# Optimization experiments

Hardware: AMD Instinct MI355X
Metric: run time of the kernel (lower is better)

## Reference

```python
import jax, jax.numpy as jnp
import numpy as np

N, E = 100000, 1600000
F_IN, H, HG, L, C = 128, 128, 128, 3, 40


def setup_inputs() -> dict:
    key = jax.random.key(0)
    ks = jax.random.split(key, 12)
    s = 0.05
    return dict(
        x=jax.random.normal(ks[0], (N, F_IN), jnp.float32),
        edge_index=jax.random.randint(ks[1], (2, E), 0, N),
        edge_weight=jax.random.uniform(ks[2], (E,), jnp.float32),
        h0=jax.random.normal(ks[3], (N, HG), jnp.float32),
        linW=jax.random.normal(ks[4], (F_IN, H), jnp.float32) * s,
        linB=jnp.zeros((H,), jnp.float32),
        convW=jax.random.normal(ks[5], (L, H, H), jnp.float32) * s,
        convB=jnp.zeros((L, H), jnp.float32),
        gru_Wih=jax.random.normal(ks[6], (3 * HG, H), jnp.float32) * s,
        gru_Whh=jax.random.normal(ks[7], (3 * HG, HG), jnp.float32) * s,
        gru_bih=jnp.zeros((3 * HG,), jnp.float32),
        gru_bhh=jnp.zeros((3 * HG,), jnp.float32),
        fcW=jax.random.normal(ks[8], (HG, C), jnp.float32) * s,
        fcB=jnp.zeros((C,), jnp.float32),
    )


def _gru(x, h, Wih, Whh, bih, bhh):
    # torch.nn.GRUCell math (gate order: r, z, n)
    gi = x @ Wih.T + bih  # [N, 3*HG]
    gh = h @ Whh.T + bhh  # [N, 3*HG]
    ir, iz, in_ = jnp.split(gi, 3, axis=-1)
    hr, hz, hn = jnp.split(gh, 3, axis=-1)
    r = jax.nn.sigmoid(ir + hr)
    z = jax.nn.sigmoid(iz + hz)
    n = jnp.tanh(in_ + r * hn)
    return (1.0 - z) * n + z * h


def _gcn_conv(x, src, dst, ew, W, b, n_nodes):
    # PyG GCNConv: linear -> symmetric-normalized sparse aggregation -> bias
    xw = x @ W  # [N, H]
    deg = jax.ops.segment_sum(ew, dst, num_segments=n_nodes)
    dinv = jnp.where(deg > 0, jax.lax.rsqrt(deg), 0.0)
    norm = dinv[src] * ew * dinv[dst]  # [E+N]
    msg = xw[src] * norm[:, None]      # gather + scale (irregular access)
    out = jax.ops.segment_sum(msg, dst, num_segments=n_nodes)  # scatter-add
    return out + b


def reference(x, edge_index, edge_weight, h0, linW, linB, convW, convB,
              gru_Wih, gru_Whh, gru_bih, gru_bhh, fcW, fcB):
    n_nodes = x.shape[0]
    # GCNConv default: add self-loops with weight 1 before normalization
    loops = jnp.arange(n_nodes)
    src = jnp.concatenate([edge_index[0], loops])
    dst = jnp.concatenate([edge_index[1], loops])
    ew = jnp.concatenate([edge_weight, jnp.ones((n_nodes,), edge_weight.dtype)])

    h = h0
    xh = jax.nn.relu(x @ linW + linB)
    h = _gru(xh, h, gru_Wih, gru_Whh, gru_bih, gru_bhh)
    for l in range(convW.shape[0]):  # fixed small layer count
        xh = jax.nn.relu(_gcn_conv(xh, src, dst, ew, convW[l], convB[l], n_nodes))
        h = _gru(xh, h, gru_Wih, gru_Whh, gru_bih, gru_bhh)
    return h @ fcW + fcB
```

## Files before the change

kernel.cpp:

```cpp
#include <hip/hip_runtime.h>
#include <hip/hip_bf16.h>
#include <math.h>

typedef __attribute__((ext_vector_type(8))) short bf8_t;
typedef __attribute__((ext_vector_type(4))) float f4_t;
typedef __attribute__((ext_vector_type(8))) unsigned short us8_t;

__device__ inline unsigned short f2bf(float f) {
  union { float f; unsigned u; } x; x.f = f;
  unsigned r = x.u + 0x7FFF + ((x.u >> 16) & 1);
  return (unsigned short)(r >> 16);
}
__device__ inline float bf2f(unsigned short b) {
  union { unsigned u; float f; } x; x.u = ((unsigned)b) << 16;
  return x.f;
}
__device__ inline float bflo(unsigned v) {
  union { unsigned u; float f; } x; x.u = v << 16; return x.f;
}
__device__ inline float bfhi(unsigned v) {
  union { unsigned u; float f; } x; x.u = v & 0xFFFF0000u; return x.f;
}

__device__ inline void async_copy16(const void* g, void* l) {
  __builtin_amdgcn_global_load_lds(
      (const __attribute__((address_space(1))) unsigned int*)g,
      (__attribute__((address_space(3))) unsigned int*)l, 16, 0, 0);
}


__global__ void k_fill1(float* __restrict__ p, int n) {
  int i = blockIdx.x * blockDim.x + threadIdx.x;
  if (i < n) p[i] = 1.0f;
}

__global__ void k_zero_i(int* __restrict__ p, int n) {
  int i = blockIdx.x * blockDim.x + threadIdx.x;
  if (i < n) p[i] = 0;
}

__global__ void k_scatter_deg(const int* __restrict__ dst, const float* __restrict__ ew,
                              float* __restrict__ deg, int E) {
  int e = blockIdx.x * blockDim.x + threadIdx.x;
  if (e < E) atomicAdd(&deg[dst[e]], ew[e]);
}

__global__ void k_count(const int* __restrict__ dst, int* __restrict__ cnt, int E) {
  int e = blockIdx.x * blockDim.x + threadIdx.x;
  if (e < E) atomicAdd(&cnt[dst[e]], 1);
}

__global__ void k_rsqrt(float* __restrict__ p, int n) {
  int i = blockIdx.x * blockDim.x + threadIdx.x;
  if (i < n) p[i] = rsqrtf(p[i]);
}

__global__ void k_f2bf(const float* __restrict__ in, unsigned short* __restrict__ out,
                       size_t n8) {
  size_t i = (size_t)blockIdx.x * blockDim.x + threadIdx.x;
  if (i >= n8) return;
  const float4* p = (const float4*)(in + i * 8);
  float4 a = p[0], b = p[1];
  us8_t v;
  v[0] = f2bf(a.x); v[1] = f2bf(a.y); v[2] = f2bf(a.z); v[3] = f2bf(a.w);
  v[4] = f2bf(b.x); v[5] = f2bf(b.y); v[6] = f2bf(b.z); v[7] = f2bf(b.w);
  *(us8_t*)(out + i * 8) = v;
}

__global__ void k_packB(const float* __restrict__ W, unsigned short* __restrict__ out,
                        int K, int Ncols, int ldw, int trans) {
  int idx = blockIdx.x * 256 + threadIdx.x;
  int total = (Ncols / 16) * (K / 32) * 64;
  if (idx >= total) return;
  int lane = idx & 63;
  int frag = idx >> 6;
  int kt = K / 32;
  int k0 = frag % kt;
  int n0 = frag / kt;
  int n = n0 * 16 + (lane & 15);
  int kbase = k0 * 32 + (lane >> 4) * 8;
  us8_t v;
#pragma unroll
  for (int j = 0; j < 8; ++j) {
    int k = kbase + j;
    float f = trans ? W[(size_t)n * ldw + k] : W[(size_t)k * ldw + n];
    v[j] = f2bf(f);
  }
  *(us8_t*)(out + (size_t)idx * 8) = v;
}


__global__ __launch_bounds__(256) void k_scan_block(
    const int* __restrict__ cnt, int* __restrict__ partial,
    int* __restrict__ bsum, int n) {
  __shared__ int s[256];
  int tid = threadIdx.x;
  int i = blockIdx.x * 256 + tid;
  s[tid] = (i < n) ? cnt[i] : 0;
  __syncthreads();
#pragma unroll
  for (int d = 1; d < 256; d <<= 1) {
    int t = (tid >= d) ? s[tid - d] : 0;
    __syncthreads();
    s[tid] += t;
    __syncthreads();
  }
  if (i < n) partial[i] = s[tid];
  if (tid == 255) bsum[blockIdx.x] = s[255];
}

__global__ __launch_bounds__(512) void k_scan_sums(int* __restrict__ bsum, int nb) {
  __shared__ int s[512];
  int tid = threadIdx.x;
  s[tid] = (tid < nb) ? bsum[tid] : 0;
  __syncthreads();
#pragma unroll
  for (int d = 1; d < 512; d <<= 1) {
    int t = (tid >= d) ? s[tid - d] : 0;
    __syncthreads();
    s[tid] += t;
    __syncthreads();
  }
  if (tid < nb) bsum[tid] = s[tid];
}

__global__ __launch_bounds__(256) void k_scan_add(
    const int* __restrict__ partial, const int* __restrict__ bsum,
    int* __restrict__ rowptr, int* __restrict__ cursor, int n) {
  int i = blockIdx.x * 256 + threadIdx.x;
  if (i == 0) { rowptr[0] = 0; cursor[0] = 0; }
  if (i < n) {
    int v = partial[i] + (blockIdx.x > 0 ? bsum[blockIdx.x - 1] : 0);
    rowptr[i + 1] = v;
    if (i + 1 < n) cursor[i + 1] = v;
  }
}

__global__ __launch_bounds__(256) void k_csr_fill(
    const int* __restrict__ src, const int* __restrict__ dst,
    const float* __restrict__ ew, const float* __restrict__ dinv,
    int* __restrict__ cursor, int2* __restrict__ csr, int E) {
  int e = blockIdx.x * 256 + threadIdx.x;
  if (e >= E) return;
  int s = src[e], d = dst[e];
  float w = dinv[s] * ew[e] * dinv[d];
  int pos = atomicAdd(&cursor[d], 1);
  csr[pos] = make_int2(s, __float_as_int(w));
}


template<bool RELU, bool BIAS>
__global__ __launch_bounds__(256) void k_mfma_gemm(
    const unsigned short* __restrict__ A, const unsigned short* __restrict__ Bp,
    const float* __restrict__ bias, unsigned short* __restrict__ C, int M) {
  __shared__ unsigned char smem[32 * 1024];
  int wave = threadIdx.x >> 6, lane = threadIdx.x & 63;
  int row0 = (blockIdx.x * 4 + wave) * 16;
  int m = lane & 15, q = lane >> 4;

#pragma unroll
  for (int i = 0; i < 8; ++i) {
    int f = wave * 8 + i;
    async_copy16((const unsigned char*)Bp + (size_t)f * 1024 + lane * 16,
                 smem + f * 1024);
  }
  __syncthreads();
  if (row0 >= M) return;

  int arow = row0 + m; if (arow >= M) arow = M - 1;
  bf8_t a[4];
#pragma unroll
  for (int k0 = 0; k0 < 4; ++k0)
    a[k0] = *(const bf8_t*)(A + (size_t)arow * 128 + k0 * 32 + q * 8);

#pragma unroll
  for (int n0 = 0; n0 < 8; ++n0) {
    f4_t acc = {};
#pragma unroll
    for (int k0 = 0; k0 < 4; ++k0) {
      bf8_t b = *(const bf8_t*)(smem + (n0 * 4 + k0) * 1024 + lane * 16);
      acc = __builtin_amdgcn_mfma_f32_16x16x32_bf16(a[k0], b, acc, 0, 0, 0);
    }
    int col = n0 * 16 + m;
    float bs = BIAS ? bias[col] : 0.f;
#pragma unroll
    for (int r = 0; r < 4; ++r) {
      int grow = row0 + q * 4 + r;
      if (grow < M) {
        float v = acc[r] + bs;
        if (RELU) v = fmaxf(v, 0.f);
        C[(size_t)grow * 128 + col] = f2bf(v);
      }
    }
  }
}


__global__ __launch_bounds__(256) void k_gru_mfma(
    const unsigned short* __restrict__ xh,
    const float* h_in,
    float* h_out,
    const unsigned short* __restrict__ Bi,
    const unsigned short* __restrict__ Bh,
    const float* __restrict__ bih, const float* __restrict__ bhh, int M) {
  __shared__ unsigned char smem[24 * 1024];
  int wave = threadIdx.x >> 6, lane = threadIdx.x & 63;
  int row0 = (blockIdx.x * 4 + wave) * 16;
  int m = lane & 15, q = lane >> 4;
  int arow = row0 + m; if (arow >= M) arow = M - 1;

  bf8_t ax[4], ah[4];
#pragma unroll
  for (int k0 = 0; k0 < 4; ++k0) {
    ax[k0] = *(const bf8_t*)(xh + (size_t)arow * 128 + k0 * 32 + q * 8);
    const float* hp = h_in + (size_t)arow * 128 + k0 * 32 + q * 8;
    float4 h0 = *(const float4*)hp;
    float4 h1 = *(const float4*)(hp + 4);
    bf8_t t;
    t[0] = (short)f2bf(h0.x); t[1] = (short)f2bf(h0.y);
    t[2] = (short)f2bf(h0.z); t[3] = (short)f2bf(h0.w);
    t[4] = (short)f2bf(h1.x); t[5] = (short)f2bf(h1.y);
    t[6] = (short)f2bf(h1.z); t[7] = (short)f2bf(h1.w);
    ah[k0] = t;
  }

  auto stage = [&](int g) {
#pragma unroll
    for (int s = 0; s < 6; ++s) {
      int cc = g + 8 * (s >= 3 ? s - 3 : s);
      const unsigned short* src = (s < 3) ? Bi : Bh;
      int f = s * 4 + wave;
      async_copy16((const unsigned char*)src + ((size_t)(cc * 4 + wave)) * 1024 + lane * 16,
                   smem + f * 1024);
    }
  };

  stage(0);
  for (int g = 0; g < 8; ++g) {
    __syncthreads();
    f4_t air = {}, aiz = {}, ain = {}, ahr = {}, ahz = {}, ahn = {};
#pragma unroll
    for (int k0 = 0; k0 < 4; ++k0) {
      bf8_t br = *(const bf8_t*)(smem + (0 * 4 + k0) * 1024 + lane * 16);
      bf8_t bz = *(const bf8_t*)(smem + (1 * 4 + k0) * 1024 + lane * 16);
      bf8_t bn = *(const bf8_t*)(smem + (2 * 4 + k0) * 1024 + lane * 16);
      bf8_t cr = *(const bf8_t*)(smem + (3 * 4 + k0) * 1024 + lane * 16);
      bf8_t cz = *(const bf8_t*)(smem + (4 * 4 + k0) * 1024 + lane * 16);
      bf8_t cn = *(const bf8_t*)(smem + (5 * 4 + k0) * 1024 + lane * 16);
      air = __builtin_amdgcn_mfma_f32_16x16x32_bf16(ax[k0], br, air, 0, 0, 0);
      aiz = __builtin_amdgcn_mfma_f32_16x16x32_bf16(ax[k0], bz, aiz, 0, 0, 0);
      ain = __builtin_amdgcn_mfma_f32_16x16x32_bf16(ax[k0], bn, ain, 0, 0, 0);
      ahr = __builtin_amdgcn_mfma_f32_16x16x32_bf16(ah[k0], cr, ahr, 0, 0, 0);
      ahz = __builtin_amdgcn_mfma_f32_16x16x32_bf16(ah[k0], cz, ahz, 0, 0, 0);
      ahn = __builtin_amdgcn_mfma_f32_16x16x32_bf16(ah[k0], cn, ahn, 0, 0, 0);
    }
    __syncthreads();
    if (g < 7) stage(g + 1);

    int col = g * 16 + m;
    float bir_ = bih[col], biz_ = bih[col + 128], bin_ = bih[col + 256];
    float bhr_ = bhh[col], bhz_ = bhh[col + 128], bhn_ = bhh[col + 256];
#pragma unroll
    for (int r = 0; r < 4; ++r) {
      int grow = row0 + q * 4 + r;
      if (grow < M) {
        float hprev = h_in[(size_t)grow * 128 + col];
        float rr = 1.f / (1.f + expf(-(air[r] + bir_ + ahr[r] + bhr_)));
        float zz = 1.f / (1.f + expf(-(aiz[r] + biz_ + ahz[r] + bhz_)));
        float nn = tanhf(ain[r] + bin_ + rr * (ahn[r] + bhn_));
        h_out[(size_t)grow * 128 + col] = (1.f - zz) * nn + zz * hprev;
      }
    }
  }
}


template<bool RELU, bool BIAS>
__global__ __launch_bounds__(256) void k_gemm128(
    const float* __restrict__ A, const float* __restrict__ B,
    const float* __restrict__ bias, float* __restrict__ C, int M, int Nc) {
  __shared__ float As[64][36];
  __shared__ float Bs[32][64];
  int tid = threadIdx.x;
  int tx = tid & 15, ty = tid >> 4;
  int row0 = blockIdx.y * 64, col0 = blockIdx.x * 64;
  float acc[4][4] = {};

  for (int k0 = 0; k0 < 128; k0 += 32) {
#pragma unroll
    for (int i = 0; i < 2; ++i) {
      int f = tid + i * 256;
      int r = f >> 3, c4 = f & 7;
      int gr = row0 + r;
      float4 v = make_float4(0.f, 0.f, 0.f, 0.f);
      if (gr < M) v = *(const float4*)(A + (size_t)gr * 128 + k0 + c4 * 4);
      *(float4*)(&As[r][c4 * 4]) = v;
    }
#pragma unroll
    for (int i = 0; i < 2; ++i) {
      int f = tid + i * 256;
      int r = f >> 4, c4 = f & 15;
      int gc = col0 + c4 * 4;
      float4 v = make_float4(0.f, 0.f, 0.f, 0.f);
      if (gc + 3 < Nc) v = *(const float4*)(B + (size_t)(k0 + r) * Nc + gc);
      *(float4*)(&Bs[r][c4 * 4]) = v;
    }
    __syncthreads();
#pragma unroll
    for (int kk = 0; kk < 32; ++kk) {
      float4 b = *(float4*)(&Bs[kk][tx * 4]);
      float a0 = As[ty * 4 + 0][kk];
      float a1 = As[ty * 4 + 1][kk];
      float a2 = As[ty * 4 + 2][kk];
      float a3 = As[ty * 4 + 3][kk];
      acc[0][0] += a0 * b.x; acc[0][1] += a0 * b.y; acc[0][2] += a0 * b.z; acc[0][3] += a0 * b.w;
      acc[1][0] += a1 * b.x; acc[1][1] += a1 * b.y; acc[1][2] += a1 * b.z; acc[1][3] += a1 * b.w;
      acc[2][0] += a2 * b.x; acc[2][1] += a2 * b.y; acc[2][2] += a2 * b.z; acc[2][3] += a2 * b.w;
      acc[3][0] += a3 * b.x; acc[3][1] += a3 * b.y; acc[3][2] += a3 * b.z; acc[3][3] += a3 * b.w;
    }
    __syncthreads();
  }

#pragma unroll
  for (int i = 0; i < 4; ++i) {
    int gr = row0 + ty * 4 + i;
    if (gr >= M) continue;
#pragma unroll
    for (int j = 0; j < 4; ++j) {
      int gc = col0 + tx * 4 + j;
      if (gc >= Nc) continue;
      float v = acc[i][j];
      if (BIAS) v += bias[gc];
      if (RELU) v = fmaxf(v, 0.f);
      C[(size_t)gr * Nc + gc] = v;
    }
  }
}


__global__ __launch_bounds__(256) void k_gather(
    const int* __restrict__ rowptr, const int2* __restrict__ csr,
    const unsigned* __restrict__ xw,
    const float* __restrict__ dinv, const float* __restrict__ bias,
    unsigned* __restrict__ out, int N) {
  int wave = threadIdx.x >> 6;
  int lane = threadIdx.x & 63;
  int node = __builtin_amdgcn_readfirstlane(blockIdx.x * 4 + wave);
  if (node >= N) return;
  int beg = __builtin_amdgcn_readfirstlane(rowptr[node]);
  int end = __builtin_amdgcn_readfirstlane(rowptr[node + 1]);

  float accl = 0.f, acch = 0.f;
  int k = beg;
  for (; k + 4 <= end; k += 4) {
    int2 e0 = csr[k], e1 = csr[k + 1], e2 = csr[k + 2], e3 = csr[k + 3];
    unsigned v0 = xw[((size_t)e0.x << 6) + lane];
    unsigned v1 = xw[((size_t)e1.x << 6) + lane];
    unsigned v2 = xw[((size_t)e2.x << 6) + lane];
    unsigned v3 = xw[((size_t)e3.x << 6) + lane];
    float w0 = __int_as_float(e0.y), w1 = __int_as_float(e1.y);
    float w2 = __int_as_float(e2.y), w3 = __int_as_float(e3.y);
    accl += bflo(v0) * w0; acch += bfhi(v0) * w0;
    accl += bflo(v1) * w1; acch += bfhi(v1) * w1;
    accl += bflo(v2) * w2; acch += bfhi(v2) * w2;
    accl += bflo(v3) * w3; acch += bfhi(v3) * w3;
  }
  for (; k < end; ++k) {
    int2 e = csr[k];
    unsigned v = xw[((size_t)e.x << 6) + lane];
    float w = __int_as_float(e.y);
    accl += bflo(v) * w; acch += bfhi(v) * w;
  }

  float di = dinv[node];
  float sn = di * di;
  unsigned vs = xw[((size_t)node << 6) + lane];
  float2 b = *(const float2*)(bias + lane * 2);
  float rl = fmaxf(accl + bflo(vs) * sn + b.x, 0.f);
  float rh = fmaxf(acch + bfhi(vs) * sn + b.y, 0.f);
  unsigned o = (unsigned)f2bf(rl) | ((unsigned)f2bf(rh) << 16);
  out[((size_t)node << 6) + lane] = o;
}


extern "C" void kernel_launch(void* const* d_in, const int* in_sizes, int n_in,
                              void* d_out, int out_size, void* d_ws, size_t ws_size,
                              hipStream_t stream) {
  const float* x    = (const float*)d_in[0];
  const int*   ei   = (const int*)d_in[1];
  const float* ew   = (const float*)d_in[2];
  const float* h0   = (const float*)d_in[3];
  const float* linW = (const float*)d_in[4];
  const float* linB = (const float*)d_in[5];
  const float* convW= (const float*)d_in[6];
  const float* convB= (const float*)d_in[7];
  const float* Wih  = (const float*)d_in[8];
  const float* Whh  = (const float*)d_in[9];
  const float* bih  = (const float*)d_in[10];
  const float* bhh  = (const float*)d_in[11];
  const float* fcW  = (const float*)d_in[12];
  const float* fcB  = (const float*)d_in[13];

  int N = in_sizes[0] / 128;
  int E = in_sizes[1] / 2;
  const int* srcI = ei;
  const int* dstI = ei + E;
  int nb = (N + 255) / 256;

  float* ws = (float*)d_ws;
  size_t off = 0;
  float* dinv = ws + off; off += (size_t)N;
  if (off & 1) off++;
  float* h    = ws + off; off += (size_t)N * 128;
  int* iws = (int*)(ws + off);
  size_t ioff = 0;
  int2* csr    = (int2*)iws; ioff += (size_t)2 * E;
  int* cnt     = iws + ioff; ioff += (size_t)N;
  int* partial = iws + ioff; ioff += (size_t)N;
  int* bsum    = iws + ioff; ioff += 512;
  int* rowptr  = iws + ioff; ioff += (size_t)N + 1;
  int* cursor  = iws + ioff; ioff += (size_t)N;
  ioff = (ioff + 3) & ~(size_t)3;
  unsigned short* usws = (unsigned short*)(iws + ioff);
  size_t uoff = 0;
  unsigned short* x_bf   = usws + uoff; uoff += (size_t)N * 128;
  unsigned short* xh_bf  = usws + uoff; uoff += (size_t)N * 128;
  unsigned short* xw_bf  = usws + uoff; uoff += (size_t)N * 128;
  unsigned short* linWp  = usws + uoff; uoff += 128 * 128;
  unsigned short* convWp = usws + uoff; uoff += 3 * 128 * 128;
  unsigned short* Bi     = usws + uoff; uoff += 384 * 128;
  unsigned short* Bh     = usws + uoff; uoff += 384 * 128;

  k_packB<<<(8 * 4 * 64 + 255) / 256, 256, 0, stream>>>(linW, linWp, 128, 128, 128, 0);
  for (int l = 0; l < 3; ++l)
    k_packB<<<(8 * 4 * 64 + 255) / 256, 256, 0, stream>>>(
        convW + (size_t)l * 128 * 128, convWp + (size_t)l * 128 * 128, 128, 128, 128, 0);
  k_packB<<<(24 * 4 * 64 + 255) / 256, 256, 0, stream>>>(Wih, Bi, 128, 384, 128, 1);
  k_packB<<<(24 * 4 * 64 + 255) / 256, 256, 0, stream>>>(Whh, Bh, 128, 384, 128, 1);

  k_f2bf<<<(int)(((size_t)N * 16 + 255) / 256), 256, 0, stream>>>(x, x_bf, (size_t)N * 16);

  k_fill1<<<nb, 256, 0, stream>>>(dinv, N);
  k_scatter_deg<<<(E + 255) / 256, 256, 0, stream>>>(dstI, ew, dinv, E);
  k_rsqrt<<<nb, 256, 0, stream>>>(dinv, N);

  k_zero_i<<<nb, 256, 0, stream>>>(cnt, N);
  k_count<<<(E + 255) / 256, 256, 0, stream>>>(dstI, cnt, E);
  k_scan_block<<<nb, 256, 0, stream>>>(cnt, partial, bsum, N);
  k_scan_sums<<<1, 512, 0, stream>>>(bsum, nb);
  k_scan_add<<<nb, 256, 0, stream>>>(partial, bsum, rowptr, cursor, N);
  k_csr_fill<<<(E + 255) / 256, 256, 0, stream>>>(
      srcI, dstI, ew, dinv, cursor, csr, E);

  int gwave = (N + 63) / 64;

  k_mfma_gemm<true, true><<<gwave, 256, 0, stream>>>(x_bf, linWp, linB, xh_bf, N);

  k_gru_mfma<<<gwave, 256, 0, stream>>>(xh_bf, h0, h, Bi, Bh, bih, bhh, N);

  int ggat = (N + 3) / 4;
  for (int l = 0; l < 3; ++l) {
    k_mfma_gemm<false, false><<<gwave, 256, 0, stream>>>(
        xh_bf, convWp + (size_t)l * 128 * 128, nullptr, xw_bf, N);
    k_gather<<<ggat, 256, 0, stream>>>(
        rowptr, csr, (const unsigned*)xw_bf, dinv, convB + (size_t)l * 128,
        (unsigned*)xh_bf, N);
    k_gru_mfma<<<gwave, 256, 0, stream>>>(xh_bf, h, h, Bi, Bh, bih, bhh, N);
  }

  dim3 g40(1, (N + 63) / 64);
  k_gemm128<false, true><<<g40, 256, 0, stream>>>(h, fcW, fcB, (float*)d_out, N, 40);
}
```

Baseline: 998.6 us.

## Build CSR without float atomics, derive degrees and norms per-row from CSR

Replaces the float atomic degree scatter and the second atomic cursor pass with a single counting pass that records each edge's slot within its destination row. The CSR fill then becomes a deterministic, atomic-free write, and the degree, rsqrt and edge normalization are computed per node by walking CSR rows. This removes one atomic-heavy pass over the edges and the cursor buffer. In exchange it adds two per-node row-walking kernels with uneven per-thread loop lengths and reuses the xw buffer as temporary storage for the slot indices.

```diff
diff --git a/kernel.cpp b/kernel.cpp
--- a/kernel.cpp
+++ b/kernel.cpp
@@ -29,30 +29,15 @@
 }
 
 
-__global__ void k_fill1(float* __restrict__ p, int n) {
-  int i = blockIdx.x * blockDim.x + threadIdx.x;
-  if (i < n) p[i] = 1.0f;
-}
-
 __global__ void k_zero_i(int* __restrict__ p, int n) {
   int i = blockIdx.x * blockDim.x + threadIdx.x;
   if (i < n) p[i] = 0;
 }
 
-__global__ void k_scatter_deg(const int* __restrict__ dst, const float* __restrict__ ew,
-                              float* __restrict__ deg, int E) {
+__global__ void k_count_pos(const int* __restrict__ dst, int* __restrict__ cnt,
+                            int* __restrict__ pos, int E) {
   int e = blockIdx.x * blockDim.x + threadIdx.x;
-  if (e < E) atomicAdd(&deg[dst[e]], ew[e]);
-}
-
-__global__ void k_count(const int* __restrict__ dst, int* __restrict__ cnt, int E) {
-  int e = blockIdx.x * blockDim.x + threadIdx.x;
-  if (e < E) atomicAdd(&cnt[dst[e]], 1);
-}
-
-__global__ void k_rsqrt(float* __restrict__ p, int n) {
-  int i = blockIdx.x * blockDim.x + threadIdx.x;
-  if (i < n) p[i] = rsqrtf(p[i]);
+  if (e < E) pos[e] = atomicAdd(&cnt[dst[e]], 1);
 }
 
 __global__ void k_f2bf(const float* __restrict__ in, unsigned short* __restrict__ out,
@@ -126,26 +111,49 @@
 
 __global__ __launch_bounds__(256) void k_scan_add(
     const int* __restrict__ partial, const int* __restrict__ bsum,
-    int* __restrict__ rowptr, int* __restrict__ cursor, int n) {
+    int* __restrict__ rowptr, int n) {
   int i = blockIdx.x * 256 + threadIdx.x;
-  if (i == 0) { rowptr[0] = 0; cursor[0] = 0; }
+  if (i == 0) rowptr[0] = 0;
   if (i < n) {
     int v = partial[i] + (blockIdx.x > 0 ? bsum[blockIdx.x - 1] : 0);
     rowptr[i + 1] = v;
-    if (i + 1 < n) cursor[i + 1] = v;
   }
 }
 
 __global__ __launch_bounds__(256) void k_csr_fill(
     const int* __restrict__ src, const int* __restrict__ dst,
-    const float* __restrict__ ew, const float* __restrict__ dinv,
-    int* __restrict__ cursor, int2* __restrict__ csr, int E) {
+    const float* __restrict__ ew, const int* __restrict__ rowptr,
+    const int* __restrict__ pos, int2* __restrict__ csr, int E) {
   int e = blockIdx.x * 256 + threadIdx.x;
   if (e >= E) return;
-  int s = src[e], d = dst[e];
-  float w = dinv[s] * ew[e] * dinv[d];
-  int pos = atomicAdd(&cursor[d], 1);
-  csr[pos] = make_int2(s, __float_as_int(w));
+  int d = dst[e];
+  int p = rowptr[d] + pos[e];
+  csr[p] = make_int2(src[e], __float_as_int(ew[e]));
+}
+
+__global__ __launch_bounds__(256) void k_deg_dinv(
+    const int* __restrict__ rowptr, const int2* __restrict__ csr,
+    float* __restrict__ dinv, int N) {
+  int n = blockIdx.x * 256 + threadIdx.x;
+  if (n >= N) return;
+  int b = rowptr[n], e = rowptr[n + 1];
+  float s = 1.0f;
+  for (int j = b; j < e; ++j) s += __int_as_float(csr[j].y);
+  dinv[n] = rsqrtf(s);
+}
+
+__global__ __launch_bounds__(256) void k_norm_csr(
+    const int* __restrict__ rowptr, int2* __restrict__ csr,
+    const float* __restrict__ dinv, int N) {
+  int n = blockIdx.x * 256 + threadIdx.x;
+  if (n >= N) return;
+  int b = rowptr[n], e = rowptr[n + 1];
+  float dn = dinv[n];
+  for (int j = b; j < e; ++j) {
+    int2 t = csr[j];
+    float w = dinv[t.x] * __int_as_float(t.y) * dn;
+    csr[j] = make_int2(t.x, __float_as_int(w));
+  }
 }
 
 
@@ -419,7 +427,6 @@
   int* partial = iws + ioff; ioff += (size_t)N;
   int* bsum    = iws + ioff; ioff += 512;
   int* rowptr  = iws + ioff; ioff += (size_t)N + 1;
-  int* cursor  = iws + ioff; ioff += (size_t)N;
   ioff = (ioff + 3) & ~(size_t)3;
   unsigned short* usws = (unsigned short*)(iws + ioff);
   size_t uoff = 0;
@@ -431,6 +438,8 @@
   unsigned short* Bi     = usws + uoff; uoff += 384 * 128;
   unsigned short* Bh     = usws + uoff; uoff += 384 * 128;
 
+  int* pos = (int*)xw_bf;
+
   k_packB<<<(8 * 4 * 64 + 255) / 256, 256, 0, stream>>>(linW, linWp, 128, 128, 128, 0);
   for (int l = 0; l < 3; ++l)
     k_packB<<<(8 * 4 * 64 + 255) / 256, 256, 0, stream>>>(
@@ -440,17 +449,16 @@
 
   k_f2bf<<<(int)(((size_t)N * 16 + 255) / 256), 256, 0, stream>>>(x, x_bf, (size_t)N * 16);
 
-  k_fill1<<<nb, 256, 0, stream>>>(dinv, N);
-  k_scatter_deg<<<(E + 255) / 256, 256, 0, stream>>>(dstI, ew, dinv, E);
-  k_rsqrt<<<nb, 256, 0, stream>>>(dinv, N);
-
   k_zero_i<<<nb, 256, 0, stream>>>(cnt, N);
-  k_count<<<(E + 255) / 256, 256, 0, stream>>>(dstI, cnt, E);
+  k_count_pos<<<(E + 255) / 256, 256, 0, stream>>>(dstI, cnt, pos, E);
   k_scan_block<<<nb, 256, 0, stream>>>(cnt, partial, bsum, N);
   k_scan_sums<<<1, 512, 0, stream>>>(bsum, nb);
-  k_scan_add<<<nb, 256, 0, stream>>>(partial, bsum, rowptr, cursor, N);
+  k_scan_add<<<nb, 256, 0, stream>>>(partial, bsum, rowptr, N);
   k_csr_fill<<<(E + 255) / 256, 256, 0, stream>>>(
-      srcI, dstI, ew, dinv, cursor, csr, E);
+      srcI, dstI, ew, rowptr, pos, csr, E);
+
+  k_deg_dinv<<<nb, 256, 0, stream>>>(rowptr, csr, dinv, N);
+  k_norm_csr<<<nb, 256, 0, stream>>>(rowptr, csr, dinv, N);
 
   int gwave = (N + 63) / 64;
 
```

Result: faster. 914.2 us (-8.5%).
